# Kernel optimization log

Measured on AMD Instinct MI355X. Metric: run time of the kernel, lower is better.

The kernel has to match this reference:

```python
import jax, jax.numpy as jnp
import numpy as np

N, E, NC, ES, NT, G = 200000, 500000, 150000, 350000, 100000, 1024
FN, FE, H, T = 133, 14, 128, 3


def _enc_params(key, prefix):
    ks = jax.random.split(key, 4)
    g = lambda k, shape, fan_in: jax.random.normal(k, shape, jnp.float32) / np.sqrt(fan_in).astype(np.float32)
    return {
        f"{prefix}_w_node": g(ks[0], (FN, H), FN),
        f"{prefix}_b_node": jnp.zeros((H,), jnp.float32),
        f"{prefix}_w_edge": g(ks[1], (FE, H), FE),
        f"{prefix}_b_edge": jnp.zeros((H,), jnp.float32),
        f"{prefix}_w_mp": g(ks[2], (T, H, H), H),
        f"{prefix}_b_mp": jnp.zeros((T, H), jnp.float32),
        f"{prefix}_w_out": g(ks[3], (H, H), H),
        f"{prefix}_b_out": jnp.zeros((H,), jnp.float32),
    }


def setup_inputs() -> dict:
    key = jax.random.key(0)
    k = lambda i: jax.random.fold_in(key, i)
    inp = {
        "x": jax.random.normal(k(0), (N, FN), jnp.float32),
        "node_weight": jax.random.uniform(k(1), (N,), jnp.float32),
        "edge_index": jax.random.randint(k(2), (2, E), 0, N),
        "edge_attr": jax.random.normal(k(3), (E, FE), jnp.float32),
        "edge_weight": jax.random.uniform(k(4), (E,), jnp.float32),
        "batch": jnp.sort(jax.random.randint(k(5), (N,), 0, G)),
        "context_nodes_mapper": jax.random.randint(k(6), (NC,), 0, N),
        "target_nodes_mapper": jax.random.randint(k(7), (NT,), 0, N),
        "combined_subgraphs": jax.random.randint(k(8), (2, ES), 0, NC),
        "subgraphs_edges_mapper": jax.random.randint(k(9), (ES,), 0, E),
        "context_edges_mask": jax.random.bernoulli(k(10), 0.7, (ES,)),
    }
    inp.update(_enc_params(k(11), "ctx"))
    inp.update(_enc_params(k(12), "tgt"))
    return inp


def wd_mpnn(x, src, dst, edge_attr, edge_weight, node_weight,
            w_node, b_node, w_edge, b_edge, w_mp, b_mp, w_out, b_out, n_nodes):
    # Weighted-edge node MPNN: gather source node states, combine with edge
    # embedding, scale by edge weight, scatter-sum onto destination nodes.
    h = jax.nn.relu(x @ w_node + b_node)                 # [n_nodes, H]
    eh = jax.nn.relu(edge_attr @ w_edge + b_edge)        # [n_edges, H]
    ew = edge_weight[:, None]
    for t in range(w_mp.shape[0]):
        msg = ew * (h[src] + eh)                         # gather [n_edges, H]
        agg = jax.ops.segment_sum(msg, dst, num_segments=n_nodes)
        h = jax.nn.relu(h + agg @ w_mp[t] + b_mp[t])
    return (h @ w_out + b_out) * node_weight[:, None]


def segment_mean(vals, seg, num_segments):
    s = jax.ops.segment_sum(vals, seg, num_segments=num_segments)
    c = jax.ops.segment_sum(jnp.ones((vals.shape[0],), vals.dtype), seg, num_segments=num_segments)
    return s / jnp.maximum(c, 1.0)[:, None]


def reference(x, node_weight, edge_index, edge_attr, edge_weight, batch,
              context_nodes_mapper, target_nodes_mapper, combined_subgraphs,
              subgraphs_edges_mapper, context_edges_mask,
              ctx_w_node, ctx_b_node, ctx_w_edge, ctx_b_edge, ctx_w_mp, ctx_b_mp, ctx_w_out, ctx_b_out,
              tgt_w_node, tgt_b_node, tgt_w_edge, tgt_b_edge, tgt_w_mp, tgt_b_mp, tgt_w_out, tgt_b_out):
    # --- context branch: gather subgraph node/edge features ---
    cx = x[context_nodes_mapper]                         # [NC, FN]
    cnw = node_weight[context_nodes_mapper]              # [NC]
    cea = edge_attr[subgraphs_edges_mapper]              # [ES, FE]
    # boolean edge mask folded into edge weights (messages scale linearly in
    # edge_weight, so zeroing masked edges == dropping them) -> jit friendly
    cew = edge_weight[subgraphs_edges_mapper] * context_edges_mask.astype(jnp.float32)
    csrc, cdst = combined_subgraphs[0], combined_subgraphs[1]
    ctx_nodes = wd_mpnn(cx, csrc, cdst, cea, cew, cnw,
                        ctx_w_node, ctx_b_node, ctx_w_edge, ctx_b_edge,
                        ctx_w_mp, ctx_b_mp, ctx_w_out, ctx_b_out, NC)
    ctx_emb = segment_mean(ctx_nodes, batch[context_nodes_mapper], G)   # [G, H]

    # --- target branch: full-graph encode, pool over target nodes ---
    full = wd_mpnn(x, edge_index[0], edge_index[1], edge_attr, edge_weight, node_weight,
                   tgt_w_node, tgt_b_node, tgt_w_edge, tgt_b_edge,
                   tgt_w_mp, tgt_b_mp, tgt_w_out, tgt_b_out, N)
    tgt_emb = segment_mean(full[target_nodes_mapper], batch[target_nodes_mapper], G)  # [G, H]

    return jnp.stack([ctx_emb, tgt_emb])                 # [2, G, H]
```

## Files before the change

### kernel.cpp

```cpp
#include <hip/hip_runtime.h>
#include <hip/hip_fp16.h>
#include <stdint.h>

#define H 128
#define FN 133
#define FE 14
#define NG 1024
#define APAD 133

typedef float v2f __attribute__((ext_vector_type(2)));

__device__ __forceinline__ uint2 pack_half4(float4 v) {
    __half2 a = __float22half2_rn(make_float2(v.x, v.y));
    __half2 b = __float22half2_rn(make_float2(v.z, v.w));
    uint2 r;
    r.x = *reinterpret_cast<unsigned int*>(&a);
    r.y = *reinterpret_cast<unsigned int*>(&b);
    return r;
}
__device__ __forceinline__ float4 unpack_half4(uint2 u) {
    __half2 a = *reinterpret_cast<__half2*>(&u.x);
    __half2 b = *reinterpret_cast<__half2*>(&u.y);
    float2 fa = __half22float2(a);
    float2 fb = __half22float2(b);
    return make_float4(fa.x, fa.y, fb.x, fb.y);
}

__global__ void k_sniff(const unsigned int* __restrict__ w, int nwords, int* __restrict__ flag) {
    __shared__ int sawFloat, sawBig;
    if (threadIdx.x == 0) { sawFloat = 0; sawBig = 0; }
    __syncthreads();
    int f = 0, bg = 0;
    for (int i = threadIdx.x; i < nwords; i += blockDim.x) {
        unsigned int v = w[i];
        if (v == 0u || v == 1u) continue;
        if (v == 0x3F800000u) f = 1; else bg = 1;
    }
    if (f) atomicOr(&sawFloat, 1);
    if (bg) atomicOr(&sawBig, 1);
    __syncthreads();
    if (threadIdx.x == 0) *flag = sawBig ? 1 : (sawFloat ? 2 : 0);
}

__device__ __forceinline__ float mask_val(const void* mask, int mm, long e) {
    if (mm == 1)      return ((const unsigned char*)mask)[e] ? 1.f : 0.f;
    else if (mm == 2) return ((const float*)mask)[e];
    else              return ((const int*)mask)[e] ? 1.f : 0.f;
}

template<bool GATHER>
__global__ __launch_bounds__(256)
void k_gemm_enc(const float* __restrict__ x, const int* __restrict__ map, int nrows,
                const float* __restrict__ w, const float* __restrict__ bias,
                float* __restrict__ hout) {
    __shared__ float w_lds[32][H];
    __shared__ float a_lds[32][APAD];
    __shared__ int   m_lds[128];
    const int tid = threadIdx.x;
    const int rbase = blockIdx.x * 128;
    if (GATHER && tid < 128) {
        int row = rbase + tid;
        m_lds[tid] = (row < nrows) ? map[row] : 0;
    }
    const int tx = tid & 15, ty = tid >> 4;
    float acc[8][8] = {};
    for (int kc = 0; kc < 5; ++kc) {
        const int k0 = kc * 32;
        __syncthreads();
        for (int i = tid; i < 32 * 32; i += 256) {
            int kk = i >> 5, c4 = i & 31;
            float4 v = make_float4(0.f, 0.f, 0.f, 0.f);
            if (k0 + kk < FN)
                v = reinterpret_cast<const float4*>(w + (size_t)(k0 + kk) * H)[c4];
            *reinterpret_cast<float4*>(&w_lds[kk][c4 * 4]) = v;
        }
        for (int i = tid; i < 128 * 32; i += 256) {
            int r = i >> 5, kk = i & 31;
            int row = rbase + r;
            float v = 0.f;
            if (row < nrows && k0 + kk < FN) {
                int sr = GATHER ? m_lds[r] : row;
                v = x[(size_t)sr * FN + k0 + kk];
            }
            a_lds[kk][r] = v;
        }
        __syncthreads();
        #pragma unroll 4
        for (int k = 0; k < 32; ++k) {
            float4 a0 = *reinterpret_cast<const float4*>(&a_lds[k][ty * 8]);
            float4 a1 = *reinterpret_cast<const float4*>(&a_lds[k][ty * 8 + 4]);
            float4 w0 = *reinterpret_cast<const float4*>(&w_lds[k][tx * 4]);
            float4 w1 = *reinterpret_cast<const float4*>(&w_lds[k][64 + tx * 4]);
            float aa[8] = {a0.x, a0.y, a0.z, a0.w, a1.x, a1.y, a1.z, a1.w};
            float ww[8] = {w0.x, w0.y, w0.z, w0.w, w1.x, w1.y, w1.z, w1.w};
            #pragma unroll
            for (int i2 = 0; i2 < 8; ++i2)
                #pragma unroll
                for (int j = 0; j < 8; ++j)
                    acc[i2][j] += aa[i2] * ww[j];
        }
    }
    float4 b0 = *reinterpret_cast<const float4*>(bias + tx * 4);
    float4 b1 = *reinterpret_cast<const float4*>(bias + 64 + tx * 4);
    float bb[8] = {b0.x, b0.y, b0.z, b0.w, b1.x, b1.y, b1.z, b1.w};
    #pragma unroll
    for (int i2 = 0; i2 < 8; ++i2) {
        int row = rbase + ty * 8 + i2;
        if (row < nrows) {
            float4 o0, o1;
            o0.x = fmaxf(acc[i2][0] + bb[0], 0.f); o0.y = fmaxf(acc[i2][1] + bb[1], 0.f);
            o0.z = fmaxf(acc[i2][2] + bb[2], 0.f); o0.w = fmaxf(acc[i2][3] + bb[3], 0.f);
            o1.x = fmaxf(acc[i2][4] + bb[4], 0.f); o1.y = fmaxf(acc[i2][5] + bb[5], 0.f);
            o1.z = fmaxf(acc[i2][6] + bb[6], 0.f); o1.w = fmaxf(acc[i2][7] + bb[7], 0.f);
            float* hp = hout + (size_t)row * H + tx * 4;
            *reinterpret_cast<float4*>(hp)      = o0;
            *reinterpret_cast<float4*>(hp + 64) = o1;
        }
    }
}

template<int MODE>
__global__ __launch_bounds__(256)
void k_hist(const int* __restrict__ dst, const float* __restrict__ edge_weight,
            const int* __restrict__ emap, const void* __restrict__ mask,
            const int* __restrict__ mmode_p, int* __restrict__ deg, int nedges) {
    int e = blockIdx.x * 256 + threadIdx.x;
    if (e >= nedges) return;
    int eo = MODE ? emap[e] : e;
    float w = edge_weight[eo];
    if (MODE) w *= mask_val(mask, *mmode_p, e);
    if (w != 0.f) atomicAdd(&deg[dst[e]], 1);
}

__global__ __launch_bounds__(256)
void k_scan1(const int* __restrict__ deg, int* __restrict__ off, int* __restrict__ bsum, int n) {
    __shared__ int tsum[256];
    const int tid = threadIdx.x;
    const int base = blockIdx.x * 1024;
    int local[4]; int s = 0;
    #pragma unroll
    for (int j = 0; j < 4; ++j) {
        int i = base + tid * 4 + j;
        local[j] = (i < n) ? deg[i] : 0;
        s += local[j];
    }
    tsum[tid] = s;
    __syncthreads();
    for (int d = 1; d < 256; d <<= 1) {
        int v = (tid >= d) ? tsum[tid - d] : 0;
        __syncthreads();
        tsum[tid] += v;
        __syncthreads();
    }
    int excl = tsum[tid] - s;
    #pragma unroll
    for (int j = 0; j < 4; ++j) {
        int i = base + tid * 4 + j;
        if (i < n) off[i] = excl;
        excl += local[j];
    }
    if (tid == 255) bsum[blockIdx.x] = tsum[255];
}

__global__ __launch_bounds__(256)
void k_scan2(int* __restrict__ bsum, int nb) {
    __shared__ int tsum[256];
    const int tid = threadIdx.x;
    int local[4]; int s = 0;
    #pragma unroll
    for (int j = 0; j < 4; ++j) {
        int i = tid * 4 + j;
        local[j] = (i < nb) ? bsum[i] : 0;
        s += local[j];
    }
    tsum[tid] = s;
    __syncthreads();
    for (int d = 1; d < 256; d <<= 1) {
        int v = (tid >= d) ? tsum[tid - d] : 0;
        __syncthreads();
        tsum[tid] += v;
        __syncthreads();
    }
    int excl = tsum[tid] - s;
    #pragma unroll
    for (int j = 0; j < 4; ++j) {
        int i = tid * 4 + j;
        if (i < nb) bsum[i] = excl;
        excl += local[j];
    }
}

__global__ __launch_bounds__(256)
void k_scan3(const int* __restrict__ bsum, int* __restrict__ off, int* __restrict__ cur, int n) {
    int i = blockIdx.x * 256 + threadIdx.x;
    if (i < n) {
        int o = off[i] + bsum[i >> 10];
        off[i] = o;
        cur[i] = o;
    }
}

template<int MODE>
__global__ __launch_bounds__(256)
void k_scatter(const int* __restrict__ src, const int* __restrict__ dst,
               const float* __restrict__ edge_weight,
               const int* __restrict__ emap, const void* __restrict__ mask,
               const int* __restrict__ mmode_p, int* __restrict__ cur,
               int2* __restrict__ epk, int2* __restrict__ epkh,
               int nedges) {
    int e = blockIdx.x * 256 + threadIdx.x;
    if (e >= nedges) return;
    int eo = MODE ? emap[e] : e;
    float w = edge_weight[eo];
    if (MODE) w *= mask_val(mask, *mmode_p, e);
    if (w != 0.f) {
        int pos = atomicAdd(&cur[dst[e]], 1);
        int wb = __float_as_int(w);
        epk[pos]  = make_int2(src[e], wb);
        epkh[pos] = make_int2(eo, wb);
    }
}

__global__ __launch_bounds__(256)
void k_msg_eh(const int* __restrict__ off, const int* __restrict__ deg,
              const int2* __restrict__ epk, const int2* __restrict__ epkh,
              const float* __restrict__ edge_attr,
              const float* __restrict__ w_edge, const float* __restrict__ b_edge,
              const float* __restrict__ h,
              __half* __restrict__ agg, __half* __restrict__ aggeh, int nnodes) {
    __shared__ float we_lds[FE * H];
    __shared__ float be_lds[H];
    for (int i = threadIdx.x; i < FE * H; i += 256) we_lds[i] = w_edge[i];
    if (threadIdx.x < H) be_lds[threadIdx.x] = b_edge[threadIdx.x];
    __syncthreads();
    const int hw = threadIdx.x >> 5;
    const int ln = threadIdx.x & 31;
    const int c  = ln * 4;
    int v = blockIdx.x * 8 + hw;
    if (v >= nnodes) return;
    v2f acc0 = {0.f, 0.f}, acc1 = {0.f, 0.f};
    v2f aeh0 = {0.f, 0.f}, aeh1 = {0.f, 0.f};
    const int o = off[v], d = deg[v];
    const float4 bev = *reinterpret_cast<const float4*>(be_lds + c);
    const v2f bev0 = {bev.x, bev.y}, bev1 = {bev.z, bev.w};
    for (int jb = 0; jb < d; jb += 32) {
        const int nn = min(32, d - jb);
        int2 m1 = make_int2(0, 0), m2 = make_int2(0, 0);
        if (ln < nn) { m1 = epk[o + jb + ln]; m2 = epkh[o + jb + ln]; }
        const int msrc = m1.x;
        const int meo  = m2.x;
        const float mw = __int_as_float(m1.y);
        for (int q = 0; q < nn; q += 2) {
            int   s0 = __shfl(msrc, q, 32);
            int   e0 = __shfl(meo,  q, 32);
            float w0 = __shfl(mw,   q, 32);
            int   s1 = __shfl(msrc, q + 1, 32);
            int   e1 = __shfl(meo,  q + 1, 32);
            float w1 = __shfl(mw,   q + 1, 32);
            if (q + 1 >= nn) { s1 = s0; e1 = e0; w1 = 0.f; }
            float4 hv0 = *reinterpret_cast<const float4*>(h + (size_t)s0 * H + c);
            float4 hv1 = *reinterpret_cast<const float4*>(h + (size_t)s1 * H + c);
            float a0 = (ln < FE) ? edge_attr[(size_t)e0 * FE + ln] : 0.f;
            float a1 = (ln < FE) ? edge_attr[(size_t)e1 * FE + ln] : 0.f;
            v2f eh00 = bev0, eh01 = bev1, eh10 = bev0, eh11 = bev1;
            #pragma unroll
            for (int k = 0; k < FE; ++k) {
                float f0 = __shfl(a0, k, 32);
                float f1 = __shfl(a1, k, 32);
                float4 wv = *reinterpret_cast<const float4*>(we_lds + k * H + c);
                v2f wva = {wv.x, wv.y}, wvb = {wv.z, wv.w};
                v2f f0v = {f0, f0}, f1v = {f1, f1};
                eh00 += f0v * wva; eh01 += f0v * wvb;
                eh10 += f1v * wva; eh11 += f1v * wvb;
            }
            v2f r00 = {w0 * fmaxf(eh00.x, 0.f), w0 * fmaxf(eh00.y, 0.f)};
            v2f r01 = {w0 * fmaxf(eh01.x, 0.f), w0 * fmaxf(eh01.y, 0.f)};
            v2f r10 = {w1 * fmaxf(eh10.x, 0.f), w1 * fmaxf(eh10.y, 0.f)};
            v2f r11 = {w1 * fmaxf(eh11.x, 0.f), w1 * fmaxf(eh11.y, 0.f)};
            aeh0 += r00 + r10; aeh1 += r01 + r11;
            v2f w0v = {w0, w0}, w1v = {w1, w1};
            acc0 += w0v * (v2f){hv0.x, hv0.y} + w1v * (v2f){hv1.x, hv1.y} + r00 + r10;
            acc1 += w0v * (v2f){hv0.z, hv0.w} + w1v * (v2f){hv1.z, hv1.w} + r01 + r11;
        }
    }
    *reinterpret_cast<uint2*>(agg   + (size_t)v * H + c) = pack_half4(make_float4(acc0.x, acc0.y, acc1.x, acc1.y));
    *reinterpret_cast<uint2*>(aggeh + (size_t)v * H + c) = pack_half4(make_float4(aeh0.x, aeh0.y, aeh1.x, aeh1.y));
}

__global__ __launch_bounds__(256)
void k_msg_csr(const int* __restrict__ off, const int* __restrict__ deg,
               const int2* __restrict__ epk, const __half* __restrict__ aggeh,
               const float* __restrict__ h, __half* __restrict__ agg, int nnodes) {
    const int hw = threadIdx.x >> 5;
    const int ln = threadIdx.x & 31;
    const int c  = ln * 4;
    int v = blockIdx.x * 8 + hw;
    if (v >= nnodes) return;
    float4 a0 = unpack_half4(*reinterpret_cast<const uint2*>(aggeh + (size_t)v * H + c));
    v2f acc0 = {a0.x, a0.y}, acc1 = {a0.z, a0.w};
    const int o = off[v], d = deg[v];
    for (int jb = 0; jb < d; jb += 32) {
        const int nn = min(32, d - jb);
        int2 meta = make_int2(0, 0);
        if (ln < nn) meta = epk[o + jb + ln];
        const int ms = meta.x;
        const float mw = __int_as_float(meta.y);
        for (int q = 0; q < nn; q += 4) {
            #pragma unroll
            for (int u = 0; u < 4; ++u) {
                int qq = q + u;
                int   s = __shfl(ms, qq, 32);
                float w = __shfl(mw, qq, 32);
                if (qq >= nn) { s = 0; w = 0.f; }
                float4 hv = *reinterpret_cast<const float4*>(h + (size_t)s * H + c);
                v2f wv = {w, w};
                acc0 += wv * (v2f){hv.x, hv.y};
                acc1 += wv * (v2f){hv.z, hv.w};
            }
        }
    }
    *reinterpret_cast<uint2*>(agg + (size_t)v * H + c) = pack_half4(make_float4(acc0.x, acc0.y, acc1.x, acc1.y));
}

__global__ __launch_bounds__(256)
void k_gemm_update(const __half* __restrict__ agg, int nrows,
                   const float* __restrict__ w, const float* __restrict__ bias,
                   float* __restrict__ h) {
    __shared__ float w_lds[32][H];
    __shared__ float a_lds[32][APAD];
    const int tid = threadIdx.x;
    const int rbase = blockIdx.x * 128;
    const int tx = tid & 15, ty = tid >> 4;
    float acc[8][8] = {};
    for (int kc = 0; kc < 4; ++kc) {
        const int k0 = kc * 32;
        __syncthreads();
        for (int i = tid; i < 1024; i += 256) {
            int kk = i >> 5, c4 = i & 31;
            *reinterpret_cast<float4*>(&w_lds[kk][c4 * 4]) =
                reinterpret_cast<const float4*>(w + (size_t)(k0 + kk) * H)[c4];
        }
        for (int i = tid; i < 1024; i += 256) {
            int r = i >> 3, f = i & 7;
            int row = rbase + r;
            float4 v = make_float4(0.f, 0.f, 0.f, 0.f);
            if (row < nrows)
                v = unpack_half4(reinterpret_cast<const uint2*>(agg + (size_t)row * H + k0)[f]);
            a_lds[f * 4 + 0][r] = v.x;
            a_lds[f * 4 + 1][r] = v.y;
            a_lds[f * 4 + 2][r] = v.z;
            a_lds[f * 4 + 3][r] = v.w;
        }
        __syncthreads();
        #pragma unroll 4
        for (int k = 0; k < 32; ++k) {
            float4 a0 = *reinterpret_cast<const float4*>(&a_lds[k][ty * 8]);
            float4 a1 = *reinterpret_cast<const float4*>(&a_lds[k][ty * 8 + 4]);
            float4 w0 = *reinterpret_cast<const float4*>(&w_lds[k][tx * 4]);
            float4 w1 = *reinterpret_cast<const float4*>(&w_lds[k][64 + tx * 4]);
            float aa[8] = {a0.x, a0.y, a0.z, a0.w, a1.x, a1.y, a1.z, a1.w};
            float ww[8] = {w0.x, w0.y, w0.z, w0.w, w1.x, w1.y, w1.z, w1.w};
            #pragma unroll
            for (int i2 = 0; i2 < 8; ++i2)
                #pragma unroll
                for (int j = 0; j < 8; ++j)
                    acc[i2][j] += aa[i2] * ww[j];
        }
    }
    float4 b0 = *reinterpret_cast<const float4*>(bias + tx * 4);
    float4 b1 = *reinterpret_cast<const float4*>(bias + 64 + tx * 4);
    float bb[8] = {b0.x, b0.y, b0.z, b0.w, b1.x, b1.y, b1.z, b1.w};
    #pragma unroll
    for (int i2 = 0; i2 < 8; ++i2) {
        int row = rbase + ty * 8 + i2;
        if (row < nrows) {
            float* hp = h + (size_t)row * H + tx * 4;
            float4 h0 = *reinterpret_cast<const float4*>(hp);
            float4 h1 = *reinterpret_cast<const float4*>(hp + 64);
            float4 o0, o1;
            o0.x = fmaxf(h0.x + acc[i2][0] + bb[0], 0.f); o0.y = fmaxf(h0.y + acc[i2][1] + bb[1], 0.f);
            o0.z = fmaxf(h0.z + acc[i2][2] + bb[2], 0.f); o0.w = fmaxf(h0.w + acc[i2][3] + bb[3], 0.f);
            o1.x = fmaxf(h1.x + acc[i2][4] + bb[4], 0.f); o1.y = fmaxf(h1.y + acc[i2][5] + bb[5], 0.f);
            o1.z = fmaxf(h1.z + acc[i2][6] + bb[6], 0.f); o1.w = fmaxf(h1.w + acc[i2][7] + bb[7], 0.f);
            *reinterpret_cast<float4*>(hp)      = o0;
            *reinterpret_cast<float4*>(hp + 64) = o1;
        }
    }
}

__global__ __launch_bounds__(256)
void k_ghist(const int* __restrict__ rowmap, const int* __restrict__ batch,
             int* __restrict__ deg_g, int nrows) {
    int r = blockIdx.x * 256 + threadIdx.x;
    if (r < nrows) atomicAdd(&deg_g[batch[rowmap[r]]], 1);
}

__global__ __launch_bounds__(256)
void k_gscan(const int* __restrict__ deg, int* __restrict__ off, int* __restrict__ cur) {
    __shared__ int tsum[256];
    const int tid = threadIdx.x;
    int local[4]; int s = 0;
    #pragma unroll
    for (int j = 0; j < 4; ++j) { local[j] = deg[tid * 4 + j]; s += local[j]; }
    tsum[tid] = s;
    __syncthreads();
    for (int d = 1; d < 256; d <<= 1) {
        int v = (tid >= d) ? tsum[tid - d] : 0;
        __syncthreads();
        tsum[tid] += v;
        __syncthreads();
    }
    int excl = tsum[tid] - s;
    #pragma unroll
    for (int j = 0; j < 4; ++j) {
        off[tid * 4 + j] = excl;
        cur[tid * 4 + j] = excl;
        excl += local[j];
    }
}

template<bool GATHER>
__global__ __launch_bounds__(256)
void k_gscatter(const int* __restrict__ rowmap, const int* __restrict__ batch,
                const float* __restrict__ nodew, int* __restrict__ cur,
                int* __restrict__ prow, float* __restrict__ pnw, int nrows) {
    int r = blockIdx.x * 256 + threadIdx.x;
    if (r >= nrows) return;
    int oid = rowmap[r];
    int g = batch[oid];
    int pos = atomicAdd(&cur[g], 1);
    prow[pos] = GATHER ? oid : r;
    pnw[pos]  = nodew[oid];
}

__global__ __launch_bounds__(256)
void k_pool(const int* __restrict__ off_g, const int* __restrict__ deg_g,
            const int* __restrict__ prow, const float* __restrict__ pnw,
            const float* __restrict__ h,
            const float* __restrict__ w, const float* __restrict__ bias,
            float* __restrict__ outp) {
    __shared__ float s_lds[4][H];
    __shared__ float ssum[H];
    __shared__ float r_lds[2][H];
    __shared__ float cg_lds[4];
    const int g = blockIdx.x;
    const int o = off_g[g], cnt = deg_g[g];
    const int wv = threadIdx.x >> 6, lane = threadIdx.x & 63;
    float ax = 0.f, ay = 0.f, cg = 0.f;
    for (int i = wv; i < cnt; i += 4) {
        int hrow = prow[o + i];
        float nw = pnw[o + i];
        float2 v = *reinterpret_cast<const float2*>(h + (size_t)hrow * H + lane * 2);
        ax += nw * v.x; ay += nw * v.y; cg += nw;
    }
    s_lds[wv][lane * 2]     = ax;
    s_lds[wv][lane * 2 + 1] = ay;
    if (lane == 0) cg_lds[wv] = cg;
    __syncthreads();
    if (threadIdx.x < H)
        ssum[threadIdx.x] = s_lds[0][threadIdx.x] + s_lds[1][threadIdx.x]
                          + s_lds[2][threadIdx.x] + s_lds[3][threadIdx.x];
    __syncthreads();
    const int c = threadIdx.x & 127, kh = threadIdx.x >> 7;
    float p = 0.f;
    #pragma unroll 8
    for (int k = 0; k < 64; ++k)
        p += ssum[kh * 64 + k] * w[(size_t)(kh * 64 + k) * H + c];
    r_lds[kh][c] = p;
    __syncthreads();
    if (threadIdx.x < H) {
        float cga = cg_lds[0] + cg_lds[1] + cg_lds[2] + cg_lds[3];
        float val = r_lds[0][c] + r_lds[1][c] + bias[c] * cga;
        outp[(size_t)g * H + c] = val / fmaxf((float)cnt, 1.f);
    }
}

extern "C" void kernel_launch(void* const* d_in, const int* in_sizes, int n_in,
                              void* d_out, int out_size, void* d_ws, size_t ws_size,
                              hipStream_t stream) {
    (void)n_in; (void)out_size; (void)ws_size;
    const float* x           = (const float*)d_in[0];
    const float* node_weight = (const float*)d_in[1];
    const int*   edge_index  = (const int*)d_in[2];
    const float* edge_attr   = (const float*)d_in[3];
    const float* edge_weight = (const float*)d_in[4];
    const int*   batch       = (const int*)d_in[5];
    const int*   cnm         = (const int*)d_in[6];
    const int*   tnm         = (const int*)d_in[7];
    const int*   csub        = (const int*)d_in[8];
    const int*   sem         = (const int*)d_in[9];
    const void*  cmask       = d_in[10];

    const float* ctx_w_node = (const float*)d_in[11];
    const float* ctx_b_node = (const float*)d_in[12];
    const float* ctx_w_edge = (const float*)d_in[13];
    const float* ctx_b_edge = (const float*)d_in[14];
    const float* ctx_w_mp   = (const float*)d_in[15];
    const float* ctx_b_mp   = (const float*)d_in[16];
    const float* ctx_w_out  = (const float*)d_in[17];
    const float* ctx_b_out  = (const float*)d_in[18];
    const float* tgt_w_node = (const float*)d_in[19];
    const float* tgt_b_node = (const float*)d_in[20];
    const float* tgt_w_edge = (const float*)d_in[21];
    const float* tgt_b_edge = (const float*)d_in[22];
    const float* tgt_w_mp   = (const float*)d_in[23];
    const float* tgt_b_mp   = (const float*)d_in[24];
    const float* tgt_w_out  = (const float*)d_in[25];
    const float* tgt_b_out  = (const float*)d_in[26];

    const int N  = in_sizes[1];
    const int E  = in_sizes[4];
    const int NC = in_sizes[6];
    const int NT = in_sizes[7];
    const int ES = in_sizes[9];
    const int NMAX = (NT > NC) ? NT : NC;

    float* out = (float*)d_out;

    char* ws = (char*)d_ws;
    float*  h     = (float*)ws;  ws += (size_t)N * H * sizeof(float);
    __half* agg   = (__half*)ws; ws += (size_t)N * H * sizeof(__half);
    __half* aggeh = (__half*)ws; ws += (size_t)N * H * sizeof(__half);
    int2*  epk    = (int2*)ws;   ws += (size_t)E * sizeof(int2);
    int2*  epkh   = (int2*)ws;   ws += (size_t)E * sizeof(int2);
    int*   deg    = (int*)ws;    ws += (size_t)N * sizeof(int);
    int*   off    = (int*)ws;    ws += (size_t)N * sizeof(int);
    int*   cur    = (int*)ws;    ws += (size_t)N * sizeof(int);
    int*   bsum   = (int*)ws;    ws += 1024 * sizeof(int);
    int*   deg_g  = (int*)ws;    ws += NG * sizeof(int);
    int*   off_g  = (int*)ws;    ws += NG * sizeof(int);
    int*   cur_g  = (int*)ws;    ws += NG * sizeof(int);
    int*   prow   = (int*)ws;    ws += (size_t)NMAX * sizeof(int);
    float* pnw    = (float*)ws;  ws += (size_t)NMAX * sizeof(float);
    int*   flag   = (int*)ws;    ws += sizeof(int);

    int nwords = ES / 4; if (nwords > 8192) nwords = 8192;
    k_sniff<<<1, 256, 0, stream>>>((const unsigned int*)cmask, nwords, flag);

    {
        const int* fsrc = edge_index;
        const int* fdst = edge_index + E;
        hipMemsetAsync(deg, 0, (size_t)N * sizeof(int), stream);
        int egrid = (E + 255) / 256;
        k_hist<0><<<egrid, 256, 0, stream>>>(fdst, edge_weight, nullptr, nullptr, nullptr, deg, E);
        int nb1 = (N + 1023) / 1024;
        k_scan1<<<nb1, 256, 0, stream>>>(deg, off, bsum, N);
        k_scan2<<<1, 256, 0, stream>>>(bsum, nb1);
        k_scan3<<<(N + 255) / 256, 256, 0, stream>>>(bsum, off, cur, N);
        k_scatter<0><<<egrid, 256, 0, stream>>>(fsrc, fdst, edge_weight, nullptr, nullptr, nullptr,
                                                cur, epk, epkh, E);
        k_gemm_enc<false><<<(N + 127) / 128, 256, 0, stream>>>(x, nullptr, N, tgt_w_node, tgt_b_node, h);
        k_msg_eh<<<(N + 7) / 8, 256, 0, stream>>>(off, deg, epk, epkh, edge_attr,
                                                  tgt_w_edge, tgt_b_edge, h, agg, aggeh, N);
        k_gemm_update<<<(N + 127) / 128, 256, 0, stream>>>(agg, N, tgt_w_mp, tgt_b_mp, h);
        for (int t = 1; t < 3; ++t) {
            k_msg_csr<<<(N + 7) / 8, 256, 0, stream>>>(off, deg, epk, aggeh, h, agg, N);
            k_gemm_update<<<(N + 127) / 128, 256, 0, stream>>>(agg, N,
                                                               tgt_w_mp + t * H * H, tgt_b_mp + t * H, h);
        }
        hipMemsetAsync(deg_g, 0, NG * sizeof(int), stream);
        k_ghist<<<(NT + 255) / 256, 256, 0, stream>>>(tnm, batch, deg_g, NT);
        k_gscan<<<1, 256, 0, stream>>>(deg_g, off_g, cur_g);
        k_gscatter<true><<<(NT + 255) / 256, 256, 0, stream>>>(tnm, batch, node_weight, cur_g, prow, pnw, NT);
        k_pool<<<NG, 256, 0, stream>>>(off_g, deg_g, prow, pnw, h, tgt_w_out, tgt_b_out,
                                       out + (size_t)NG * H);
    }

    {
        const int* csrc = csub;
        const int* cdst = csub + ES;
        hipMemsetAsync(deg, 0, (size_t)NC * sizeof(int), stream);
        int egrid = (ES + 255) / 256;
        k_hist<1><<<egrid, 256, 0, stream>>>(cdst, edge_weight, sem, cmask, flag, deg, ES);
        int nb1 = (NC + 1023) / 1024;
        k_scan1<<<nb1, 256, 0, stream>>>(deg, off, bsum, NC);
        k_scan2<<<1, 256, 0, stream>>>(bsum, nb1);
        k_scan3<<<(NC + 255) / 256, 256, 0, stream>>>(bsum, off, cur, NC);
        k_scatter<1><<<egrid, 256, 0, stream>>>(csrc, cdst, edge_weight, sem, cmask, flag,
                                                cur, epk, epkh, ES);
        k_gemm_enc<true><<<(NC + 127) / 128, 256, 0, stream>>>(x, cnm, NC, ctx_w_node, ctx_b_node, h);
        k_msg_eh<<<(NC + 7) / 8, 256, 0, stream>>>(off, deg, epk, epkh, edge_attr,
                                                   ctx_w_edge, ctx_b_edge, h, agg, aggeh, NC);
        k_gemm_update<<<(NC + 127) / 128, 256, 0, stream>>>(agg, NC, ctx_w_mp, ctx_b_mp, h);
        for (int t = 1; t < 3; ++t) {
            k_msg_csr<<<(NC + 7) / 8, 256, 0, stream>>>(off, deg, epk, aggeh, h, agg, NC);
            k_gemm_update<<<(NC + 127) / 128, 256, 0, stream>>>(agg, NC,
                                                                ctx_w_mp + t * H * H, ctx_b_mp + t * H, h);
        }
        hipMemsetAsync(deg_g, 0, NG * sizeof(int), stream);
        k_ghist<<<(NC + 255) / 256, 256, 0, stream>>>(cnm, batch, deg_g, NC);
        k_gscan<<<1, 256, 0, stream>>>(deg_g, off_g, cur_g);
        k_gscatter<false><<<(NC + 255) / 256, 256, 0, stream>>>(cnm, batch, node_weight, cur_g, prow, pnw, NC);
        k_pool<<<NG, 256, 0, stream>>>(off_g, deg_g, prow, pnw, h, ctx_w_out, ctx_b_out, out);
    }
}
```

Measured before the change: 1.526 ms.

## Use fp16 MFMA for node encoder GEMM instead of scalar FMA

Rewrites the node-feature encoder GEMM (x @ w_node) to stage A and W tiles in LDS as fp16 and compute with 16x16x32 f16 MFMA instructions on each wavefront, in place of an 8x8 per-thread fp32 outer-product. This targets the ALU cost of the 133x128 projection over up to 200k rows. In exchange it lowers input precision to fp16 and moves to scalar, strided output stores.

```diff
diff --git a/kernel.cpp b/kernel.cpp
--- a/kernel.cpp
+++ b/kernel.cpp
@@ -9,6 +9,8 @@
 #define APAD 133
 
 typedef float v2f __attribute__((ext_vector_type(2)));
+typedef _Float16 f16x8 __attribute__((ext_vector_type(8)));
+typedef float f32x4 __attribute__((ext_vector_type(4)));
 
 __device__ __forceinline__ uint2 pack_half4(float4 v) {
     __half2 a = __float22half2_rn(make_float2(v.x, v.y));
@@ -53,27 +55,21 @@
 void k_gemm_enc(const float* __restrict__ x, const int* __restrict__ map, int nrows,
                 const float* __restrict__ w, const float* __restrict__ bias,
                 float* __restrict__ hout) {
-    __shared__ float w_lds[32][H];
-    __shared__ float a_lds[32][APAD];
-    __shared__ int   m_lds[128];
+    __shared__ _Float16 a_lds[128][40];
+    __shared__ _Float16 w_lds[128][40];
+    __shared__ int m_lds[128];
     const int tid = threadIdx.x;
     const int rbase = blockIdx.x * 128;
     if (GATHER && tid < 128) {
         int row = rbase + tid;
         m_lds[tid] = (row < nrows) ? map[row] : 0;
     }
-    const int tx = tid & 15, ty = tid >> 4;
-    float acc[8][8] = {};
+    const int lane = tid & 63, wv = tid >> 6;
+    const int lrow = lane & 15, kgrp = lane >> 4;
+    f32x4 acc[2][8] = {};
     for (int kc = 0; kc < 5; ++kc) {
         const int k0 = kc * 32;
         __syncthreads();
-        for (int i = tid; i < 32 * 32; i += 256) {
-            int kk = i >> 5, c4 = i & 31;
-            float4 v = make_float4(0.f, 0.f, 0.f, 0.f);
-            if (k0 + kk < FN)
-                v = reinterpret_cast<const float4*>(w + (size_t)(k0 + kk) * H)[c4];
-            *reinterpret_cast<float4*>(&w_lds[kk][c4 * 4]) = v;
-        }
         for (int i = tid; i < 128 * 32; i += 256) {
             int r = i >> 5, kk = i & 31;
             int row = rbase + r;
@@ -82,39 +78,37 @@
                 int sr = GATHER ? m_lds[r] : row;
                 v = x[(size_t)sr * FN + k0 + kk];
             }
-            a_lds[kk][r] = v;
-        }
-        __syncthreads();
-        #pragma unroll 4
-        for (int k = 0; k < 32; ++k) {
-            float4 a0 = *reinterpret_cast<const float4*>(&a_lds[k][ty * 8]);
-            float4 a1 = *reinterpret_cast<const float4*>(&a_lds[k][ty * 8 + 4]);
-            float4 w0 = *reinterpret_cast<const float4*>(&w_lds[k][tx * 4]);
-            float4 w1 = *reinterpret_cast<const float4*>(&w_lds[k][64 + tx * 4]);
-            float aa[8] = {a0.x, a0.y, a0.z, a0.w, a1.x, a1.y, a1.z, a1.w};
-            float ww[8] = {w0.x, w0.y, w0.z, w0.w, w1.x, w1.y, w1.z, w1.w};
-            #pragma unroll
-            for (int i2 = 0; i2 < 8; ++i2)
+            a_lds[r][kk] = (_Float16)v;
+        }
+        for (int i = tid; i < 32 * 128; i += 256) {
+            int kk = i >> 7, col = i & 127;
+            float v = (k0 + kk < FN) ? w[(size_t)(k0 + kk) * H + col] : 0.f;
+            w_lds[col][kk] = (_Float16)v;
+        }
+        __syncthreads();
+        f16x8 af0 = *reinterpret_cast<const f16x8*>(&a_lds[wv * 32 + lrow][kgrp * 8]);
+        f16x8 af1 = *reinterpret_cast<const f16x8*>(&a_lds[wv * 32 + 16 + lrow][kgrp * 8]);
+        #pragma unroll
+        for (int ct = 0; ct < 8; ++ct) {
+            f16x8 bf = *reinterpret_cast<const f16x8*>(&w_lds[ct * 16 + lrow][kgrp * 8]);
+            acc[0][ct] = __builtin_amdgcn_mfma_f32_16x16x32_f16(af0, bf, acc[0][ct], 0, 0, 0);
+            acc[1][ct] = __builtin_amdgcn_mfma_f32_16x16x32_f16(af1, bf, acc[1][ct], 0, 0, 0);
+        }
+    }
+    float bcol[8];
+    #pragma unroll
+    for (int ct = 0; ct < 8; ++ct) bcol[ct] = bias[ct * 16 + lrow];
+    #pragma unroll
+    for (int rt = 0; rt < 2; ++rt) {
+        #pragma unroll
+        for (int j = 0; j < 4; ++j) {
+            int row = rbase + wv * 32 + rt * 16 + kgrp * 4 + j;
+            if (row < nrows) {
+                float* hp = hout + (size_t)row * H + lrow;
                 #pragma unroll
-                for (int j = 0; j < 8; ++j)
-                    acc[i2][j] += aa[i2] * ww[j];
-        }
-    }
-    float4 b0 = *reinterpret_cast<const float4*>(bias + tx * 4);
-    float4 b1 = *reinterpret_cast<const float4*>(bias + 64 + tx * 4);
-    float bb[8] = {b0.x, b0.y, b0.z, b0.w, b1.x, b1.y, b1.z, b1.w};
-    #pragma unroll
-    for (int i2 = 0; i2 < 8; ++i2) {
-        int row = rbase + ty * 8 + i2;
-        if (row < nrows) {
-            float4 o0, o1;
-            o0.x = fmaxf(acc[i2][0] + bb[0], 0.f); o0.y = fmaxf(acc[i2][1] + bb[1], 0.f);
-            o0.z = fmaxf(acc[i2][2] + bb[2], 0.f); o0.w = fmaxf(acc[i2][3] + bb[3], 0.f);
-            o1.x = fmaxf(acc[i2][4] + bb[4], 0.f); o1.y = fmaxf(acc[i2][5] + bb[5], 0.f);
-            o1.z = fmaxf(acc[i2][6] + bb[6], 0.f); o1.w = fmaxf(acc[i2][7] + bb[7], 0.f);
-            float* hp = hout + (size_t)row * H + tx * 4;
-            *reinterpret_cast<float4*>(hp)      = o0;
-            *reinterpret_cast<float4*>(hp + 64) = o1;
+                for (int ct = 0; ct < 8; ++ct)
+                    hp[ct * 16] = fmaxf(acc[rt][ct][j] + bcol[ct], 0.f);
+            }
         }
     }
 }
```

Result: no change. 1.548 ms (+1.4%).

## Restrict final target-branch message pass and update to pooled target nodes

Applied to the files above, without the earlier changes.

The target branch only pools the final hidden states of target nodes. So the last message-passing step and its GEMM update now run only over a compacted list of the distinct nodes named in target_nodes_mapper. A mark kernel flags those nodes and a ballot-based compaction builds the list. The msg and update kernels gain a LIST template path that indexes through it, cutting roughly half the work of the final iteration. This adds two small kernels, a memset and indirect row addressing, and it launches full-size grids whose blocks early-exit against a device-side count.

```diff
diff --git a/kernel.cpp b/kernel.cpp
--- a/kernel.cpp
+++ b/kernel.cpp
@@ -218,6 +218,29 @@
         int wb = __float_as_int(w);
         epk[pos]  = make_int2(src[e], wb);
         epkh[pos] = make_int2(eo, wb);
+    }
+}
+
+__global__ __launch_bounds__(256)
+void k_mark(const int* __restrict__ rowmap, int* __restrict__ nflag, int nrows) {
+    int r = blockIdx.x * 256 + threadIdx.x;
+    if (r < nrows) nflag[rowmap[r]] = 1;
+}
+
+__global__ __launch_bounds__(256)
+void k_compact(const int* __restrict__ nflag, int* __restrict__ list,
+               int* __restrict__ cnt, int n) {
+    int i = blockIdx.x * 256 + threadIdx.x;
+    bool p = (i < n) && (nflag[i] != 0);
+    unsigned long long m = __ballot(p);
+    int lane = threadIdx.x & 63;
+    int wcount = __popcll(m);
+    int base = 0;
+    if (lane == 0 && wcount) base = atomicAdd(cnt, wcount);
+    base = __shfl(base, 0, 64);
+    if (p) {
+        int pos = base + (int)__popcll(m & ((1ull << lane) - 1ull));
+        list[pos] = i;
     }
 }
 
@@ -287,15 +310,20 @@
     *reinterpret_cast<uint2*>(aggeh + (size_t)v * H + c) = pack_half4(make_float4(aeh0.x, aeh0.y, aeh1.x, aeh1.y));
 }
 
+template<int LIST>
 __global__ __launch_bounds__(256)
 void k_msg_csr(const int* __restrict__ off, const int* __restrict__ deg,
                const int2* __restrict__ epk, const __half* __restrict__ aggeh,
-               const float* __restrict__ h, __half* __restrict__ agg, int nnodes) {
+               const float* __restrict__ h, __half* __restrict__ agg,
+               const int* __restrict__ list, const int* __restrict__ cnt_p,
+               int nnodes) {
     const int hw = threadIdx.x >> 5;
     const int ln = threadIdx.x & 31;
     const int c  = ln * 4;
-    int v = blockIdx.x * 8 + hw;
-    if (v >= nnodes) return;
+    int i = blockIdx.x * 8 + hw;
+    int bound = LIST ? *cnt_p : nnodes;
+    if (i >= bound) return;
+    int v = LIST ? list[i] : i;
     float4 a0 = unpack_half4(*reinterpret_cast<const uint2*>(aggeh + (size_t)v * H + c));
     v2f acc0 = {a0.x, a0.y}, acc1 = {a0.z, a0.w};
     const int o = off[v], d = deg[v];
@@ -322,14 +350,23 @@
     *reinterpret_cast<uint2*>(agg + (size_t)v * H + c) = pack_half4(make_float4(acc0.x, acc0.y, acc1.x, acc1.y));
 }
 
+template<int LIST>
 __global__ __launch_bounds__(256)
 void k_gemm_update(const __half* __restrict__ agg, int nrows,
                    const float* __restrict__ w, const float* __restrict__ bias,
-                   float* __restrict__ h) {
+                   float* __restrict__ h,
+                   const int* __restrict__ list, const int* __restrict__ cnt_p) {
     __shared__ float w_lds[32][H];
     __shared__ float a_lds[32][APAD];
+    __shared__ int   m_lds[128];
     const int tid = threadIdx.x;
     const int rbase = blockIdx.x * 128;
+    const int bound = LIST ? *cnt_p : nrows;
+    if (rbase >= bound) return;
+    if (LIST && tid < 128) {
+        int r = rbase + tid;
+        m_lds[tid] = (r < bound) ? list[r] : 0;
+    }
     const int tx = tid & 15, ty = tid >> 4;
     float acc[8][8] = {};
     for (int kc = 0; kc < 4; ++kc) {
@@ -344,8 +381,10 @@
             int r = i >> 3, f = i & 7;
             int row = rbase + r;
             float4 v = make_float4(0.f, 0.f, 0.f, 0.f);
-            if (row < nrows)
-                v = unpack_half4(reinterpret_cast<const uint2*>(agg + (size_t)row * H + k0)[f]);
+            if (row < bound) {
+                int hr = LIST ? m_lds[r] : row;
+                v = unpack_half4(reinterpret_cast<const uint2*>(agg + (size_t)hr * H + k0)[f]);
+            }
             a_lds[f * 4 + 0][r] = v.x;
             a_lds[f * 4 + 1][r] = v.y;
             a_lds[f * 4 + 2][r] = v.z;
@@ -373,8 +412,9 @@
     #pragma unroll
     for (int i2 = 0; i2 < 8; ++i2) {
         int row = rbase + ty * 8 + i2;
-        if (row < nrows) {
-            float* hp = h + (size_t)row * H + tx * 4;
+        if (row < bound) {
+            int hr = LIST ? m_lds[ty * 8 + i2] : row;
+            float* hp = h + (size_t)hr * H + tx * 4;
             float4 h0 = *reinterpret_cast<const float4*>(hp);
             float4 h1 = *reinterpret_cast<const float4*>(hp + 64);
             float4 o0, o1;
@@ -526,6 +566,9 @@
     int*   deg    = (int*)ws;    ws += (size_t)N * sizeof(int);
     int*   off    = (int*)ws;    ws += (size_t)N * sizeof(int);
     int*   cur    = (int*)ws;    ws += (size_t)N * sizeof(int);
+    int*   nflag  = (int*)ws;    ws += (size_t)N * sizeof(int);
+    int*   ncnt   = (int*)ws;    ws += sizeof(int);
+    int*   nlist  = (int*)ws;    ws += (size_t)N * sizeof(int);
     int*   bsum   = (int*)ws;    ws += 1024 * sizeof(int);
     int*   deg_g  = (int*)ws;    ws += NG * sizeof(int);
     int*   off_g  = (int*)ws;    ws += NG * sizeof(int);
@@ -541,6 +584,7 @@
         const int* fsrc = edge_index;
         const int* fdst = edge_index + E;
         hipMemsetAsync(deg, 0, (size_t)N * sizeof(int), stream);
+        hipMemsetAsync(nflag, 0, ((size_t)N + 1) * sizeof(int), stream);
         int egrid = (E + 255) / 256;
         k_hist<0><<<egrid, 256, 0, stream>>>(fdst, edge_weight, nullptr, nullptr, nullptr, deg, E);
         int nb1 = (N + 1023) / 1024;
@@ -549,15 +593,20 @@
         k_scan3<<<(N + 255) / 256, 256, 0, stream>>>(bsum, off, cur, N);
         k_scatter<0><<<egrid, 256, 0, stream>>>(fsrc, fdst, edge_weight, nullptr, nullptr, nullptr,
                                                 cur, epk, epkh, E);
+        k_mark<<<(NT + 255) / 256, 256, 0, stream>>>(tnm, nflag, NT);
+        k_compact<<<(N + 255) / 256, 256, 0, stream>>>(nflag, nlist, ncnt, N);
+
         k_gemm_enc<false><<<(N + 127) / 128, 256, 0, stream>>>(x, nullptr, N, tgt_w_node, tgt_b_node, h);
         k_msg_eh<<<(N + 7) / 8, 256, 0, stream>>>(off, deg, epk, epkh, edge_attr,
                                                   tgt_w_edge, tgt_b_edge, h, agg, aggeh, N);
-        k_gemm_update<<<(N + 127) / 128, 256, 0, stream>>>(agg, N, tgt_w_mp, tgt_b_mp, h);
-        for (int t = 1; t < 3; ++t) {
-            k_msg_csr<<<(N + 7) / 8, 256, 0, stream>>>(off, deg, epk, aggeh, h, agg, N);
-            k_gemm_update<<<(N + 127) / 128, 256, 0, stream>>>(agg, N,
-                                                               tgt_w_mp + t * H * H, tgt_b_mp + t * H, h);
-        }
+        k_gemm_update<0><<<(N + 127) / 128, 256, 0, stream>>>(agg, N, tgt_w_mp, tgt_b_mp, h,
+                                                              nullptr, nullptr);
+        k_msg_csr<0><<<(N + 7) / 8, 256, 0, stream>>>(off, deg, epk, aggeh, h, agg, nullptr, nullptr, N);
+        k_gemm_update<0><<<(N + 127) / 128, 256, 0, stream>>>(agg, N, tgt_w_mp + H * H, tgt_b_mp + H, h,
+                                                              nullptr, nullptr);
+        k_msg_csr<1><<<(N + 7) / 8, 256, 0, stream>>>(off, deg, epk, aggeh, h, agg, nlist, ncnt, N);
+        k_gemm_update<1><<<(N + 127) / 128, 256, 0, stream>>>(agg, N, tgt_w_mp + 2 * H * H, tgt_b_mp + 2 * H, h,
+                                                              nlist, ncnt);
         hipMemsetAsync(deg_g, 0, NG * sizeof(int), stream);
         k_ghist<<<(NT + 255) / 256, 256, 0, stream>>>(tnm, batch, deg_g, NT);
         k_gscan<<<1, 256, 0, stream>>>(deg_g, off_g, cur_g);
@@ -581,11 +630,13 @@
         k_gemm_enc<true><<<(NC + 127) / 128, 256, 0, stream>>>(x, cnm, NC, ctx_w_node, ctx_b_node, h);
         k_msg_eh<<<(NC + 7) / 8, 256, 0, stream>>>(off, deg, epk, epkh, edge_attr,
                                                    ctx_w_edge, ctx_b_edge, h, agg, aggeh, NC);
-        k_gemm_update<<<(NC + 127) / 128, 256, 0, stream>>>(agg, NC, ctx_w_mp, ctx_b_mp, h);
+        k_gemm_update<0><<<(NC + 127) / 128, 256, 0, stream>>>(agg, NC, ctx_w_mp, ctx_b_mp, h,
+                                                               nullptr, nullptr);
         for (int t = 1; t < 3; ++t) {
-            k_msg_csr<<<(NC + 7) / 8, 256, 0, stream>>>(off, deg, epk, aggeh, h, agg, NC);
-            k_gemm_update<<<(NC + 127) / 128, 256, 0, stream>>>(agg, NC,
-                                                                ctx_w_mp + t * H * H, ctx_b_mp + t * H, h);
+            k_msg_csr<0><<<(NC + 7) / 8, 256, 0, stream>>>(off, deg, epk, aggeh, h, agg, nullptr, nullptr, NC);
+            k_gemm_update<0><<<(NC + 127) / 128, 256, 0, stream>>>(agg, NC,
+                                                                   ctx_w_mp + t * H * H, ctx_b_mp + t * H, h,
+                                                                   nullptr, nullptr);
         }
         hipMemsetAsync(deg_g, 0, NG * sizeof(int), stream);
         k_ghist<<<(NC + 255) / 256, 256, 0, stream>>>(cnm, batch, deg_g, NC);
```

Measured after the change: 1.499 ms. About the same (-1.8%).
